# Performance work log

Hardware: AMD Instinct MI355X
Metric: run time of the kernel (lower is better)

Reference implementation:

```python
import jax, jax.numpy as jnp
import numpy as np

N_NODES = 100000
N_EDGES = 1600000
F_IN = 256
DIM = 32
N_CLASSES = 40


def setup_inputs() -> dict:
    key = jax.random.key(0)
    ks = jax.random.split(key, 8)
    x = jax.random.normal(ks[0], (N_NODES, F_IN), dtype=jnp.float32)
    edge_index = jax.random.randint(ks[1], (2, N_EDGES), 0, N_NODES, dtype=jnp.int64)
    s1 = 1.0 / np.sqrt(F_IN)
    s2 = 1.0 / np.sqrt(DIM)
    return {
        "x": x,
        "edge_index": edge_index,
        # SAGEConv layer 1: lin_l (aggregated neighbors, with bias) + lin_r (root)
        "W1l": jax.random.uniform(ks[2], (F_IN, DIM), jnp.float32, -s1, s1),
        "W1r": jax.random.uniform(ks[3], (F_IN, DIM), jnp.float32, -s1, s1),
        "b1": jnp.zeros((DIM,), jnp.float32),
        # SAGEConv layer 2
        "W2l": jax.random.uniform(ks[4], (DIM, N_CLASSES), jnp.float32, -s2, s2),
        "W2r": jax.random.uniform(ks[5], (DIM, N_CLASSES), jnp.float32, -s2, s2),
        "b2": jnp.zeros((N_CLASSES,), jnp.float32),
    }


def reference(x, edge_index, W1l, W1r, b1, W2l, W2r, b2):
    N = x.shape[0]
    src, dst = edge_index[0], edge_index[1]
    # in-degree for mean aggregation (clamped to avoid div-by-zero, matching
    # PyG mean-scatter semantics where isolated nodes get zeros)
    deg = jax.ops.segment_sum(jnp.ones_like(src, dtype=x.dtype), dst, num_segments=N)
    inv_deg = (1.0 / jnp.maximum(deg, 1.0))[:, None]  # [N,1]

    def sage_conv(h, Wl, Wr, b):
        # mean over incoming neighbor features, then linear + root linear
        agg = jax.ops.segment_sum(h[src], dst, num_segments=N) * inv_deg  # [N,F]
        return agg @ Wl + h @ Wr + b

    h = jax.nn.relu(sage_conv(x, W1l, W1r, b1))
    # F.dropout(p=0.5, training=self.training): identity in eval mode
    h = sage_conv(h, W2l, W2r, b2)
    return jax.nn.log_softmax(h, axis=1)
```

## Files before the change

kernel.cpp:

```cpp
#include <hip/hip_runtime.h>
#include <hip/hip_bf16.h>
#include <math.h>

#define N_NODES 100000
#define N_EDGES 1600000
#define F_IN 256
#define DIM 32
#define NC 40
#define NCP 48

#define NBLK 391

#define NPART 8
#define FPART_SZ 12500
#define FILL_BLOCKS 2048
#define PROJ_BLOCKS 1563
#define FAT_GRID 4096

typedef _Float16 half_t;
typedef _Float16 h8 __attribute__((ext_vector_type(8)));
typedef float f32x4 __attribute__((ext_vector_type(4)));
union H8 { float4 f4; half_t h[8]; };

__global__ void deg_kernel(const int* __restrict__ dst, int* __restrict__ degi) {
    int i = blockIdx.x * blockDim.x + threadIdx.x;
    if (i < N_EDGES) atomicAdd(&degi[dst[i]], 1);
}

__device__ __forceinline__ int block_scan_excl(int v, int& tot) {
    int lane = threadIdx.x & 63;
    int wid = threadIdx.x >> 6;
    int s = v;
#pragma unroll
    for (int off = 1; off < 64; off <<= 1) {
        int t = __shfl_up(s, off, 64);
        if (lane >= off) s += t;
    }
    __shared__ int wsum[8];
    if (lane == 63) wsum[wid] = s;
    __syncthreads();
    int nw = (blockDim.x + 63) >> 6;
    int wprev = 0, total = 0;
    for (int i = 0; i < nw; ++i) {
        int t = wsum[i];
        if (i < wid) wprev += t;
        total += t;
    }
    tot = total;
    return wprev + s - v;
}

__global__ void scanA_kernel(const int* __restrict__ degi, int* __restrict__ partial) {
    int i = blockIdx.x * 256 + threadIdx.x;
    int v = (i < N_NODES) ? degi[i] : 0;
    int tot;
    block_scan_excl(v, tot);
    if (threadIdx.x == 0) partial[blockIdx.x] = tot;
}

__global__ void scanB_kernel(int* __restrict__ partial, int* __restrict__ blockoff) {
    int i = threadIdx.x;
    int v = (i < NBLK) ? partial[i] : 0;
    int tot;
    int ex = block_scan_excl(v, tot);
    if (i < NBLK) blockoff[i] = ex;
}

__global__ void scanC_kernel(const int* __restrict__ degi,
                             const int* __restrict__ blockoff,
                             int* __restrict__ rowstart,
                             int* __restrict__ cursor) {
    int i = blockIdx.x * 256 + threadIdx.x;
    int v = (i < N_NODES) ? degi[i] : 0;
    int tot;
    int ex = block_scan_excl(v, tot) + blockoff[blockIdx.x];
    if (i < N_NODES) {
        rowstart[i] = ex;
        cursor[i] = ex;
    }
}

__global__ void wconv1(const float* __restrict__ W1l,
                       const float* __restrict__ W1r,
                       half_t* __restrict__ Wt) {
    int i = blockIdx.x * 256 + threadIdx.x;
    if (i >= 64 * F_IN) return;
    int c = i >> 8;
    int k = i & 255;
    float v = (c < DIM) ? W1l[(size_t)k * DIM + c] : W1r[(size_t)k * DIM + (c - DIM)];
    Wt[i] = (half_t)v;
}

__global__ void wconv2(const float* __restrict__ W2l,
                       const float* __restrict__ W2r,
                       half_t* __restrict__ Wt2l,
                       half_t* __restrict__ Wt2r) {
    int i = blockIdx.x * 256 + threadIdx.x;
    if (i >= 2 * NCP * DIM) return;
    int tab = i >= NCP * DIM;
    int j = i - tab * NCP * DIM;
    int c = j >> 5;
    int k = j & 31;
    const float* W = tab ? W2r : W2l;
    half_t* T = tab ? Wt2r : Wt2l;
    float v = (c < NC) ? W[(size_t)k * NC + c] : 0.f;
    T[j] = (half_t)v;
}

__device__ __forceinline__ void fill_body(int fid,
                                          const int* __restrict__ src,
                                          const int* __restrict__ dst,
                                          int* __restrict__ cursor,
                                          int* __restrict__ csr) {
    int x = fid & (NPART - 1);
    int gblk = fid >> 3;
    int tid = gblk * 256 + threadIdx.x;
    int stride = (FILL_BLOCKS >> 3) * 256;
    int lo = x * FPART_SZ;
    int hi = (x == NPART - 1) ? N_NODES : lo + FPART_SZ;

    const int4* dst4 = (const int4*)dst;
    for (int e4 = tid; e4 < N_EDGES / 4; e4 += stride) {
        int4 d4 = dst4[e4];
        int e = e4 * 4;
#pragma unroll
        for (int c = 0; c < 4; ++c) {
            int d = (c == 0) ? d4.x : (c == 1) ? d4.y : (c == 2) ? d4.z : d4.w;
            if (d >= lo && d < hi) {
                int pos = atomicAdd(&cursor[d], 1);
                csr[pos] = src[e + c];
            }
        }
    }
}

__device__ __forceinline__ void proj_body(int pid,
                                          const float* __restrict__ x,
                                          const half_t* __restrict__ Wt,
                                          half_t* __restrict__ P1h,
                                          half_t* __restrict__ R1h) {
    __shared__ half_t xs[64][136];
    int t = threadIdx.x;
    int wid = t >> 6;
    int lane = t & 63;
    int n0 = pid * 64;

    int arow = lane & 15;
    int kb = lane >> 4;
    int r = wid * 16 + arow;
    int nvalid = N_NODES - n0;
    const half_t* wb = Wt + (size_t)arow * F_IN + kb * 8;

    f32x4 acc[4];
#pragma unroll
    for (int ct = 0; ct < 4; ++ct) acc[ct] = (f32x4){0.f, 0.f, 0.f, 0.f};

#pragma unroll
    for (int kc = 0; kc < 2; ++kc) {
#pragma unroll
        for (int i = 0; i < 8; ++i) {
            int vidx = t + 256 * i;
            int row = vidx >> 5;
            int c4 = vidx & 31;
            int ldrow = (row < nvalid) ? row : 0;
            float4 v = *((const float4*)(x + (size_t)(n0 + ldrow) * F_IN + kc * 128) + c4);
            half_t* dsts = &xs[row][c4 * 4];
            dsts[0] = (half_t)v.x; dsts[1] = (half_t)v.y;
            dsts[2] = (half_t)v.z; dsts[3] = (half_t)v.w;
        }
        __syncthreads();
#pragma unroll
        for (int kk = 0; kk < 128; kk += 32) {
            h8 af = *(const h8*)&xs[r][kb * 8 + kk];
            int kg = kc * 128 + kk;
#pragma unroll
            for (int ct = 0; ct < 4; ++ct) {
                h8 bf = *(const h8*)&wb[(size_t)ct * 16 * F_IN + kg];
                acc[ct] = __builtin_amdgcn_mfma_f32_16x16x32_f16(af, bf, acc[ct], 0, 0, 0);
            }
        }
        __syncthreads();
    }

    int jrow = (lane >> 4) * 4;
    int cc = lane & 15;
    int nw0 = n0 + wid * 16;
#pragma unroll
    for (int ct = 0; ct < 4; ++ct) {
        int cglob = ct * 16 + cc;
        half_t* outp = (cglob < DIM) ? (P1h + cglob) : (R1h + (cglob - DIM));
#pragma unroll
        for (int j = 0; j < 4; ++j) {
            int n = nw0 + jrow + j;
            if (n < N_NODES) outp[(size_t)n * DIM] = (half_t)acc[ct][j];
        }
    }
}

__global__ __launch_bounds__(256)
void fill_proj_kernel(const int* __restrict__ src,
                      const int* __restrict__ dst,
                      int* __restrict__ cursor,
                      int* __restrict__ csr,
                      const float* __restrict__ x,
                      const half_t* __restrict__ Wt,
                      half_t* __restrict__ P1h,
                      half_t* __restrict__ R1h) {
    int chunk = blockIdx.x >> 5;
    int r = blockIdx.x & 31;
    if (r < 16) {
        int fid = chunk * 16 + r;
        if (fid < FILL_BLOCKS) fill_body(fid, src, dst, cursor, csr);
    } else {
        int pid = chunk * 16 + (r - 16);
        if (pid < PROJ_BLOCKS) proj_body(pid, x, Wt, P1h, R1h);
    }
}

__device__ __forceinline__ void gather_node(const int* __restrict__ csr,
                                            const half_t* __restrict__ feat,
                                            int rs, int re, int q8, float acc[8]) {
#pragma unroll
    for (int i = 0; i < 8; ++i) acc[i] = 0.f;
    int e = rs;
    for (; e + 2 <= re; e += 2) {
        int s0 = csr[e];
        int s1 = csr[e + 1];
        H8 u0, u1;
        u0.f4 = *(const float4*)&feat[(size_t)s0 * DIM + q8];
        u1.f4 = *(const float4*)&feat[(size_t)s1 * DIM + q8];
#pragma unroll
        for (int i = 0; i < 8; ++i) acc[i] += (float)u0.h[i] + (float)u1.h[i];
    }
    if (e < re) {
        int s0 = csr[e];
        H8 u0;
        u0.f4 = *(const float4*)&feat[(size_t)s0 * DIM + q8];
#pragma unroll
        for (int i = 0; i < 8; ++i) acc[i] += (float)u0.h[i];
    }
}

__global__ __launch_bounds__(256)
void agg1_h_kernel(const int* __restrict__ rowstart,
                   const int* __restrict__ degi,
                   const int* __restrict__ csr,
                   const half_t* __restrict__ P1h,
                   const half_t* __restrict__ R1h,
                   const float* __restrict__ b1,
                   half_t* __restrict__ h) {
    int wave = blockIdx.x * 4 + (threadIdx.x >> 6);
    int lane = threadIdx.x & 63;
    int node = wave * 16 + (lane >> 2);
    if (node >= N_NODES) return;
    int q8 = (lane & 3) * 8;
    int rs = rowstart[node];
    int dg = degi[node];
    float acc[8];
    gather_node(csr, P1h, rs, rs + dg, q8, acc);
    float inv = 1.0f / (float)max(dg, 1);
    H8 r;
    r.f4 = *(const float4*)&R1h[(size_t)node * DIM + q8];
    float4 bb0 = *(const float4*)&b1[q8];
    float4 bb1 = *(const float4*)&b1[q8 + 4];
    float rb[8] = { (float)r.h[0] + bb0.x, (float)r.h[1] + bb0.y,
                    (float)r.h[2] + bb0.z, (float)r.h[3] + bb0.w,
                    (float)r.h[4] + bb1.x, (float)r.h[5] + bb1.y,
                    (float)r.h[6] + bb1.z, (float)r.h[7] + bb1.w };
    H8 o;
#pragma unroll
    for (int i = 0; i < 8; ++i) {
        float v = fmaf(acc[i], inv, rb[i]);
        o.h[i] = (half_t)(v > 0.f ? v : 0.f);
    }
    *(float4*)&h[(size_t)node * DIM + q8] = o.f4;
}

__global__ __launch_bounds__(256)
void agg2_kernel(const int* __restrict__ rowstart,
                 const int* __restrict__ degi,
                 const int* __restrict__ csr,
                 const half_t* __restrict__ h,
                 half_t* __restrict__ a2h) {
    int wave = blockIdx.x * 4 + (threadIdx.x >> 6);
    int lane = threadIdx.x & 63;
    int node = wave * 16 + (lane >> 2);
    if (node >= N_NODES) return;
    int q8 = (lane & 3) * 8;
    int rs = rowstart[node];
    int dg = degi[node];
    float acc[8];
    gather_node(csr, h, rs, rs + dg, q8, acc);
    float inv = 1.0f / (float)max(dg, 1);
    H8 o;
#pragma unroll
    for (int i = 0; i < 8; ++i) o.h[i] = (half_t)(acc[i] * inv);
    *(float4*)&a2h[(size_t)node * DIM + q8] = o.f4;
}

__global__ __launch_bounds__(256)
void out_mfma(const half_t* __restrict__ a2h,
              const half_t* __restrict__ h,
              const half_t* __restrict__ Wt2l,
              const half_t* __restrict__ Wt2r,
              const float* __restrict__ b2,
              float* __restrict__ out) {
    int wid = threadIdx.x >> 6;
    int lane = threadIdx.x & 63;
    int n0 = blockIdx.x * 64 + wid * 16;
    if (n0 >= N_NODES) return;

    int arow = lane & 15;
    int kb = lane >> 4;
    int node = n0 + arow;
    int ldnode = node < N_NODES ? node : N_NODES - 1;

    h8 afA = *(const h8*)&a2h[(size_t)ldnode * DIM + kb * 8];
    h8 afH = *(const h8*)&h[(size_t)ldnode * DIM + kb * 8];

    f32x4 acc[3];
#pragma unroll
    for (int ct = 0; ct < 3; ++ct) {
        const h8 bl = *(const h8*)&Wt2l[(size_t)(ct * 16 + arow) * DIM + kb * 8];
        const h8 br = *(const h8*)&Wt2r[(size_t)(ct * 16 + arow) * DIM + kb * 8];
        f32x4 a = (f32x4){0.f, 0.f, 0.f, 0.f};
        a = __builtin_amdgcn_mfma_f32_16x16x32_f16(afA, bl, a, 0, 0, 0);
        a = __builtin_amdgcn_mfma_f32_16x16x32_f16(afH, br, a, 0, 0, 0);
        acc[ct] = a;
    }

    int cc = lane & 15;
#pragma unroll
    for (int ct = 0; ct < 3; ++ct) {
        int cglob = ct * 16 + cc;
        float bias = (cglob < NC) ? b2[cglob] : -1e30f;
#pragma unroll
        for (int j = 0; j < 4; ++j)
            acc[ct][j] = (cglob < NC) ? acc[ct][j] + bias : -1e30f;
    }

    float lg[4];
#pragma unroll
    for (int j = 0; j < 4; ++j) {
        float m = fmaxf(fmaxf(acc[0][j], acc[1][j]), acc[2][j]);
#pragma unroll
        for (int mk = 1; mk < 16; mk <<= 1)
            m = fmaxf(m, __shfl_xor(m, mk, 64));
        float s = __expf(acc[0][j] - m) + __expf(acc[1][j] - m) + __expf(acc[2][j] - m);
#pragma unroll
        for (int mk = 1; mk < 16; mk <<= 1)
            s += __shfl_xor(s, mk, 64);
        lg[j] = m + __logf(s);
    }

    int jrow = (lane >> 4) * 4;
#pragma unroll
    for (int ct = 0; ct < 3; ++ct) {
        int cglob = ct * 16 + cc;
        if (cglob < NC) {
#pragma unroll
            for (int j = 0; j < 4; ++j) {
                int n = n0 + jrow + j;
                if (n < N_NODES) out[(size_t)n * NC + cglob] = acc[ct][j] - lg[j];
            }
        }
    }
}

extern "C" void kernel_launch(void* const* d_in, const int* in_sizes, int n_in,
                              void* d_out, int out_size, void* d_ws, size_t ws_size,
                              hipStream_t stream) {
    const float* x   = (const float*)d_in[0];
    const int*   ei  = (const int*)d_in[1];
    const float* W1l = (const float*)d_in[2];
    const float* W1r = (const float*)d_in[3];
    const float* b1  = (const float*)d_in[4];
    const float* W2l = (const float*)d_in[5];
    const float* W2r = (const float*)d_in[6];
    const float* b2  = (const float*)d_in[7];
    float* out = (float*)d_out;

    const int* src = ei;
    const int* dst = ei + N_EDGES;

    char* ws = (char*)d_ws;
    int*    degi     = (int*)ws;      ws += sizeof(int) * 102400;
    int*    rowstart = (int*)ws;      ws += sizeof(int) * 102400;
    int*    cursor   = (int*)ws;      ws += sizeof(int) * 102400;
    int*    partial  = (int*)ws;      ws += sizeof(int) * 512;
    int*    blockoff = (int*)ws;      ws += sizeof(int) * 512;
    int*    csr      = (int*)ws;      ws += sizeof(int) * N_EDGES;
    half_t* P1h      = (half_t*)ws;   ws += sizeof(half_t) * N_NODES * DIM;
    half_t* h        = (half_t*)ws;   ws += sizeof(half_t) * N_NODES * DIM;
    half_t* a2h      = (half_t*)ws;   ws += sizeof(half_t) * N_NODES * DIM;
    half_t* R1h      = (half_t*)ws;   ws += sizeof(half_t) * N_NODES * DIM;
    half_t* Wt       = (half_t*)ws;   ws += sizeof(half_t) * 64 * F_IN;
    half_t* Wt2l     = (half_t*)ws;   ws += sizeof(half_t) * NCP * DIM;
    half_t* Wt2r     = (half_t*)ws;   ws += sizeof(half_t) * NCP * DIM;

    hipMemsetAsync(degi, 0, sizeof(int) * 102400, stream);

    wconv1<<<64, 256, 0, stream>>>(W1l, W1r, Wt);
    wconv2<<<12, 256, 0, stream>>>(W2l, W2r, Wt2l, Wt2r);
    deg_kernel<<<(N_EDGES + 255) / 256, 256, 0, stream>>>(dst, degi);
    scanA_kernel<<<NBLK, 256, 0, stream>>>(degi, partial);
    scanB_kernel<<<1, 512, 0, stream>>>(partial, blockoff);
    scanC_kernel<<<NBLK, 256, 0, stream>>>(degi, blockoff, rowstart, cursor);

    fill_proj_kernel<<<FAT_GRID, 256, 0, stream>>>(src, dst, cursor, csr,
                                                   x, Wt, P1h, R1h);

    int gather_blocks = (N_NODES + 63) / 64;
    agg1_h_kernel<<<gather_blocks, 256, 0, stream>>>(rowstart, degi, csr, P1h, R1h, b1, h);
    agg2_kernel<<<gather_blocks, 256, 0, stream>>>(rowstart, degi, csr, h, a2h);
    out_mfma<<<(N_NODES + 63) / 64, 256, 0, stream>>>(a2h, h, Wt2l, Wt2r, b2, out);
}
```

Baseline: 365.5 us.

## Fuse weight conversion with degree count, drop scanB, fuse agg2 with output MFMA

The two weight-conversion kernels are merged with degree counting into one launch. The separate block-offset scan is removed by having each scanC block sum the preceding partials itself. The second-layer gather now writes its mean into shared memory and feeds the MFMA output stage in the same kernel, which drops the a2h global round trip and one launch. The gather loop is unrolled to four edges to expose more memory-level parallelism. The fused fill/projection grid is split into two half launches, which adds a launch and changes how fill and projection blocks overlap.

Measured after the change: 352.5 us. 3.5% less time.

```diff
diff --git a/kernel.cpp b/kernel.cpp
--- a/kernel.cpp
+++ b/kernel.cpp
@@ -15,16 +15,42 @@
 #define FPART_SZ 12500
 #define FILL_BLOCKS 2048
 #define PROJ_BLOCKS 1563
-#define FAT_GRID 4096
 
 typedef _Float16 half_t;
 typedef _Float16 h8 __attribute__((ext_vector_type(8)));
 typedef float f32x4 __attribute__((ext_vector_type(4)));
 union H8 { float4 f4; half_t h[8]; };
 
-__global__ void deg_kernel(const int* __restrict__ dst, int* __restrict__ degi) {
-    int i = blockIdx.x * blockDim.x + threadIdx.x;
-    if (i < N_EDGES) atomicAdd(&degi[dst[i]], 1);
+__global__ __launch_bounds__(256)
+void wdeg_kernel(const int* __restrict__ dst, int* __restrict__ degi,
+                 const float* __restrict__ W1l, const float* __restrict__ W1r,
+                 half_t* __restrict__ Wt,
+                 const float* __restrict__ W2l, const float* __restrict__ W2r,
+                 half_t* __restrict__ Wt2l, half_t* __restrict__ Wt2r) {
+    int b = blockIdx.x;
+    int t = threadIdx.x;
+    if (b < 64) {
+        int i = b * 256 + t;
+        int c = i >> 8;
+        int k = i & 255;
+        float v = (c < DIM) ? W1l[(size_t)k * DIM + c] : W1r[(size_t)k * DIM + (c - DIM)];
+        Wt[i] = (half_t)v;
+    } else if (b < 76) {
+        int i = (b - 64) * 256 + t;
+        if (i < 2 * NCP * DIM) {
+            int tab = i >= NCP * DIM;
+            int j = i - tab * NCP * DIM;
+            int c = j >> 5;
+            int k = j & 31;
+            const float* W = tab ? W2r : W2l;
+            half_t* T = tab ? Wt2r : Wt2l;
+            float v = (c < NC) ? W[(size_t)k * NC + c] : 0.f;
+            T[j] = (half_t)v;
+        }
+    } else {
+        int i = (b - 76) * 256 + t;
+        if (i < N_EDGES) atomicAdd(&degi[dst[i]], 1);
+    }
 }
 
 __device__ __forceinline__ int block_scan_excl(int v, int& tot) {
@@ -58,53 +84,31 @@
     if (threadIdx.x == 0) partial[blockIdx.x] = tot;
 }
 
-__global__ void scanB_kernel(int* __restrict__ partial, int* __restrict__ blockoff) {
-    int i = threadIdx.x;
-    int v = (i < NBLK) ? partial[i] : 0;
-    int tot;
-    int ex = block_scan_excl(v, tot);
-    if (i < NBLK) blockoff[i] = ex;
-}
-
 __global__ void scanC_kernel(const int* __restrict__ degi,
-                             const int* __restrict__ blockoff,
+                             const int* __restrict__ partial,
                              int* __restrict__ rowstart,
                              int* __restrict__ cursor) {
-    int i = blockIdx.x * 256 + threadIdx.x;
+    int t = threadIdx.x;
+    int b = blockIdx.x;
+    int s = (t < b) ? partial[t] : 0;
+    int i1 = t + 256;
+    if (i1 < b) s += partial[i1];
+#pragma unroll
+    for (int off = 1; off < 64; off <<= 1) s += __shfl_xor(s, off, 64);
+    __shared__ int ws2[4];
+    if ((t & 63) == 0) ws2[t >> 6] = s;
+    __syncthreads();
+    int boff = ws2[0] + ws2[1] + ws2[2] + ws2[3];
+    __syncthreads();
+
+    int i = b * 256 + t;
     int v = (i < N_NODES) ? degi[i] : 0;
     int tot;
-    int ex = block_scan_excl(v, tot) + blockoff[blockIdx.x];
+    int ex = block_scan_excl(v, tot) + boff;
     if (i < N_NODES) {
         rowstart[i] = ex;
         cursor[i] = ex;
     }
-}
-
-__global__ void wconv1(const float* __restrict__ W1l,
-                       const float* __restrict__ W1r,
-                       half_t* __restrict__ Wt) {
-    int i = blockIdx.x * 256 + threadIdx.x;
-    if (i >= 64 * F_IN) return;
-    int c = i >> 8;
-    int k = i & 255;
-    float v = (c < DIM) ? W1l[(size_t)k * DIM + c] : W1r[(size_t)k * DIM + (c - DIM)];
-    Wt[i] = (half_t)v;
-}
-
-__global__ void wconv2(const float* __restrict__ W2l,
-                       const float* __restrict__ W2r,
-                       half_t* __restrict__ Wt2l,
-                       half_t* __restrict__ Wt2r) {
-    int i = blockIdx.x * 256 + threadIdx.x;
-    if (i >= 2 * NCP * DIM) return;
-    int tab = i >= NCP * DIM;
-    int j = i - tab * NCP * DIM;
-    int c = j >> 5;
-    int k = j & 31;
-    const float* W = tab ? W2r : W2l;
-    half_t* T = tab ? Wt2r : Wt2l;
-    float v = (c < NC) ? W[(size_t)k * NC + c] : 0.f;
-    T[j] = (half_t)v;
 }
 
 __device__ __forceinline__ void fill_body(int fid,
@@ -205,14 +209,15 @@
                       const float* __restrict__ x,
                       const half_t* __restrict__ Wt,
                       half_t* __restrict__ P1h,
-                      half_t* __restrict__ R1h) {
+                      half_t* __restrict__ R1h,
+                      int fbase, int pbase) {
     int chunk = blockIdx.x >> 5;
     int r = blockIdx.x & 31;
     if (r < 16) {
-        int fid = chunk * 16 + r;
-        if (fid < FILL_BLOCKS) fill_body(fid, src, dst, cursor, csr);
+        int fid = fbase + chunk * 16 + r;
+        fill_body(fid, src, dst, cursor, csr);
     } else {
-        int pid = chunk * 16 + (r - 16);
+        int pid = pbase + chunk * 16 + (r - 16);
         if (pid < PROJ_BLOCKS) proj_body(pid, x, Wt, P1h, R1h);
     }
 }
@@ -223,16 +228,21 @@
 #pragma unroll
     for (int i = 0; i < 8; ++i) acc[i] = 0.f;
     int e = rs;
-    for (; e + 2 <= re; e += 2) {
+    for (; e + 4 <= re; e += 4) {
         int s0 = csr[e];
         int s1 = csr[e + 1];
-        H8 u0, u1;
+        int s2 = csr[e + 2];
+        int s3 = csr[e + 3];
+        H8 u0, u1, u2, u3;
         u0.f4 = *(const float4*)&feat[(size_t)s0 * DIM + q8];
         u1.f4 = *(const float4*)&feat[(size_t)s1 * DIM + q8];
-#pragma unroll
-        for (int i = 0; i < 8; ++i) acc[i] += (float)u0.h[i] + (float)u1.h[i];
-    }
-    if (e < re) {
+        u2.f4 = *(const float4*)&feat[(size_t)s2 * DIM + q8];
+        u3.f4 = *(const float4*)&feat[(size_t)s3 * DIM + q8];
+#pragma unroll
+        for (int i = 0; i < 8; ++i)
+            acc[i] += ((float)u0.h[i] + (float)u1.h[i]) + ((float)u2.h[i] + (float)u3.h[i]);
+    }
+    for (; e < re; ++e) {
         int s0 = csr[e];
         H8 u0;
         u0.f4 = *(const float4*)&feat[(size_t)s0 * DIM + q8];
@@ -277,45 +287,47 @@
 }
 
 __global__ __launch_bounds__(256)
-void agg2_kernel(const int* __restrict__ rowstart,
-                 const int* __restrict__ degi,
-                 const int* __restrict__ csr,
-                 const half_t* __restrict__ h,
-                 half_t* __restrict__ a2h) {
-    int wave = blockIdx.x * 4 + (threadIdx.x >> 6);
-    int lane = threadIdx.x & 63;
-    int node = wave * 16 + (lane >> 2);
-    if (node >= N_NODES) return;
-    int q8 = (lane & 3) * 8;
-    int rs = rowstart[node];
-    int dg = degi[node];
-    float acc[8];
-    gather_node(csr, h, rs, rs + dg, q8, acc);
-    float inv = 1.0f / (float)max(dg, 1);
-    H8 o;
-#pragma unroll
-    for (int i = 0; i < 8; ++i) o.h[i] = (half_t)(acc[i] * inv);
-    *(float4*)&a2h[(size_t)node * DIM + q8] = o.f4;
-}
-
-__global__ __launch_bounds__(256)
-void out_mfma(const half_t* __restrict__ a2h,
+void agg2_out(const int* __restrict__ rowstart,
+              const int* __restrict__ degi,
+              const int* __restrict__ csr,
               const half_t* __restrict__ h,
               const half_t* __restrict__ Wt2l,
               const half_t* __restrict__ Wt2r,
               const float* __restrict__ b2,
               float* __restrict__ out) {
-    int wid = threadIdx.x >> 6;
-    int lane = threadIdx.x & 63;
-    int n0 = blockIdx.x * 64 + wid * 16;
-    if (n0 >= N_NODES) return;
+    __shared__ half_t a2s[64][40];
+    int t = threadIdx.x;
+    int wid = t >> 6;
+    int lane = t & 63;
+    int n0 = blockIdx.x * 64;
+
+    int nrow = wid * 16 + (lane >> 2);
+    int node = n0 + nrow;
+    int q8 = (lane & 3) * 8;
+    H8 o;
+    if (node < N_NODES) {
+        int rs = rowstart[node];
+        int dg = degi[node];
+        float acc[8];
+        gather_node(csr, h, rs, rs + dg, q8, acc);
+        float inv = 1.0f / (float)max(dg, 1);
+#pragma unroll
+        for (int i = 0; i < 8; ++i) o.h[i] = (half_t)(acc[i] * inv);
+    } else {
+#pragma unroll
+        for (int i = 0; i < 8; ++i) o.h[i] = (half_t)0.f;
+    }
+    *(float4*)&a2s[nrow][q8] = o.f4;
+    __syncthreads();
 
     int arow = lane & 15;
     int kb = lane >> 4;
-    int node = n0 + arow;
-    int ldnode = node < N_NODES ? node : N_NODES - 1;
-
-    h8 afA = *(const h8*)&a2h[(size_t)ldnode * DIM + kb * 8];
+    int mrow = wid * 16 + arow;
+    int mbase = n0 + wid * 16;
+    int mnode = mbase + arow;
+    int ldnode = mnode < N_NODES ? mnode : N_NODES - 1;
+
+    h8 afA = *(const h8*)&a2s[mrow][kb * 8];
     h8 afH = *(const h8*)&h[(size_t)ldnode * DIM + kb * 8];
 
     f32x4 acc[3];
@@ -360,7 +372,7 @@
         if (cglob < NC) {
 #pragma unroll
             for (int j = 0; j < 4; ++j) {
-                int n = n0 + jrow + j;
+                int n = mbase + jrow + j;
                 if (n < N_NODES) out[(size_t)n * NC + cglob] = acc[ct][j] - lg[j];
             }
         }
@@ -388,11 +400,9 @@
     int*    rowstart = (int*)ws;      ws += sizeof(int) * 102400;
     int*    cursor   = (int*)ws;      ws += sizeof(int) * 102400;
     int*    partial  = (int*)ws;      ws += sizeof(int) * 512;
-    int*    blockoff = (int*)ws;      ws += sizeof(int) * 512;
     int*    csr      = (int*)ws;      ws += sizeof(int) * N_EDGES;
     half_t* P1h      = (half_t*)ws;   ws += sizeof(half_t) * N_NODES * DIM;
     half_t* h        = (half_t*)ws;   ws += sizeof(half_t) * N_NODES * DIM;
-    half_t* a2h      = (half_t*)ws;   ws += sizeof(half_t) * N_NODES * DIM;
     half_t* R1h      = (half_t*)ws;   ws += sizeof(half_t) * N_NODES * DIM;
     half_t* Wt       = (half_t*)ws;   ws += sizeof(half_t) * 64 * F_IN;
     half_t* Wt2l     = (half_t*)ws;   ws += sizeof(half_t) * NCP * DIM;
@@ -400,18 +410,18 @@
 
     hipMemsetAsync(degi, 0, sizeof(int) * 102400, stream);
 
-    wconv1<<<64, 256, 0, stream>>>(W1l, W1r, Wt);
-    wconv2<<<12, 256, 0, stream>>>(W2l, W2r, Wt2l, Wt2r);
-    deg_kernel<<<(N_EDGES + 255) / 256, 256, 0, stream>>>(dst, degi);
+    wdeg_kernel<<<6326, 256, 0, stream>>>(dst, degi, W1l, W1r, Wt,
+                                          W2l, W2r, Wt2l, Wt2r);
     scanA_kernel<<<NBLK, 256, 0, stream>>>(degi, partial);
-    scanB_kernel<<<1, 512, 0, stream>>>(partial, blockoff);
-    scanC_kernel<<<NBLK, 256, 0, stream>>>(degi, blockoff, rowstart, cursor);
-
-    fill_proj_kernel<<<FAT_GRID, 256, 0, stream>>>(src, dst, cursor, csr,
-                                                   x, Wt, P1h, R1h);
-
-    int gather_blocks = (N_NODES + 63) / 64;
-    agg1_h_kernel<<<gather_blocks, 256, 0, stream>>>(rowstart, degi, csr, P1h, R1h, b1, h);
-    agg2_kernel<<<gather_blocks, 256, 0, stream>>>(rowstart, degi, csr, h, a2h);
-    out_mfma<<<(N_NODES + 63) / 64, 256, 0, stream>>>(a2h, h, Wt2l, Wt2r, b2, out);
-}
+    scanC_kernel<<<NBLK, 256, 0, stream>>>(degi, partial, rowstart, cursor);
+
+    fill_proj_kernel<<<2048, 256, 0, stream>>>(src, dst, cursor, csr,
+                                               x, Wt, P1h, R1h, 0, 0);
+    fill_proj_kernel<<<2048, 256, 0, stream>>>(src, dst, cursor, csr,
+                                               x, Wt, P1h, R1h, 1024, 1024);
+
+    agg1_h_kernel<<<(N_NODES + 63) / 64, 256, 0, stream>>>(rowstart, degi, csr,
+                                                           P1h, R1h, b1, h);
+    agg2_out<<<(N_NODES + 63) / 64, 256, 0, stream>>>(rowstart, degi, csr, h,
+                                                      Wt2l, Wt2r, b2, out);
+}
```
